# Optimization experiments

Measured on AMD Instinct MI355X. Metric: run time of the kernel, lower is better.

The kernel has to match this reference:

```python
import jax, jax.numpy as jnp
import numpy as np

B, E, L = 8, 512, 8192
MAX_W = 4          # max_subword_block_width -> widths 1..3
KSIZE = 5          # conv_kernel_size
DS = 2             # downsample_rate


def setup_inputs() -> dict:
    key = jax.random.key(0)
    k0, k1, k2, k3 = jax.random.split(key, 4)
    x = jax.random.normal(k0, (B, E, L), dtype=jnp.float32)
    # Conv1d(E, E, KSIZE): weight [out_ch, in_ch, k], bias [out_ch]
    conv_w = jax.random.normal(k1, (E, E, KSIZE), dtype=jnp.float32) * (1.0 / np.sqrt(E * KSIZE))
    conv_b = jax.random.normal(k2, (E,), dtype=jnp.float32) * 0.01
    # Linear(E, 1, bias=False): stored as vector [E]
    score_w = jax.random.normal(k3, (E,), dtype=jnp.float32) * (1.0 / np.sqrt(E))
    return {"x": x, "conv_w": conv_w, "conv_b": conv_b, "score_w": score_w}


def reference(x, conv_w, conv_b, score_w):
    length = x.shape[-1]  # original length, captured BEFORE the valid conv (as in torch)
    # Pre-GBST conv, VALID padding -> length shrinks by KSIZE-1
    y = jax.lax.conv_general_dilated(
        x, conv_w, window_strides=(1,), padding="VALID",
        dimension_numbers=("NCH", "OIH", "NCH"))
    y = y + conv_b[None, :, None]

    seqs, scs = [], []
    for w in range(1, MAX_W):
        Lc = y.shape[-1]
        pad = (-Lc) % w
        yp = jnp.pad(y, ((0, 0), (0, 0), (0, pad))) if pad else y
        # avg_pool1d(kernel=w, stride=w) == reshape + mean (zero-pad counts in mean, matching torch)
        cand = yp.reshape(yp.shape[0], yp.shape[1], -1, w).mean(-1)  # [B,E,Nb]
        sc = jnp.einsum("ben,e->bn", cand, score_w)                  # [B,Nb]
        rs = jnp.repeat(cand, w, axis=-1)  # [B,E,Nb*w]
        rc = jnp.repeat(sc, w, axis=-1)    # [B,Nb*w]
        Lr = rs.shape[-1]
        if Lr < length:
            rs = jnp.pad(rs, ((0, 0), (0, 0), (0, length - Lr)))
            rc = jnp.pad(rc, ((0, 0), (0, length - Lr)))
        seqs.append(rs[:, :, :length])
        scs.append(rc[:, :length])
    seqs = jnp.stack(seqs, axis=-1)            # [B,E,L,W-1]
    scs = jnp.stack(scs, axis=-1)[:, None]     # [B,1,L,W-1]
    att = jax.nn.softmax(scs, axis=-1)
    out = (seqs * att).sum(-1)                 # [B,E,L]
    # Downsample via avg_pool1d(kernel=DS, stride=DS)
    b, e, l = out.shape
    out = out[:, :, :(l // DS) * DS].reshape(b, e, l // DS, DS).mean(-1)
    return out
```

## Files before the change

### kernel.cpp

```cpp
#include <hip/hip_runtime.h>
#include <math.h>

#define B_    8
#define E_    512
#define L_    8192
#define K_    5
#define LC    8188
#define LOUT  4096
#define XROWS 8200
#define LCP   8208


typedef float  f32x4   __attribute__((ext_vector_type(4)));
typedef float  f32x16  __attribute__((ext_vector_type(16)));
typedef short  s16x4   __attribute__((ext_vector_type(4)));
typedef short  s16x8   __attribute__((ext_vector_type(8)));

__device__ __forceinline__ unsigned short f2bf(float f) {
    union { float f; unsigned u; } v; v.f = f;
    unsigned r = v.u + 0x7FFFu + ((v.u >> 16) & 1u);
    return (unsigned short)(r >> 16);
}
__device__ __forceinline__ float bflo(unsigned u) {
    union { unsigned u; float f; } v; v.u = u << 16; return v.f;
}
__device__ __forceinline__ float bfhi(unsigned u) {
    union { unsigned u; float f; } v; v.u = u & 0xFFFF0000u; return v.f;
}

__global__ __launch_bounds__(256) void wt_kernel(const float* __restrict__ w,
                                                 unsigned short* __restrict__ Wtb) {
    int idx = blockIdx.x * 256 + threadIdx.x;
    if (idx >= E_ * E_ * K_) return;
    int i    = idx & (E_ - 1);
    int rest = idx >> 9;
    int e    = rest & (E_ - 1);
    int k    = rest >> 9;
    Wtb[idx] = f2bf(w[((size_t)e * E_ + i) * K_ + k]);
}

__global__ __launch_bounds__(256) void xt_kernel(const float* __restrict__ x,
                                                 unsigned short* __restrict__ xT) {
    __shared__ float s[64][65];
    const int b  = blockIdx.z;
    const int i0 = blockIdx.y * 64;
    const int t0 = blockIdx.x * 64;
    #pragma unroll
    for (int j = 0; j < 4; ++j) {
        int idx = threadIdx.x + j * 256;
        int r = idx >> 4, c4 = idx & 15;
        f32x4 v = *(const f32x4*)(x + ((size_t)b * E_ + i0 + r) * L_ + t0 + c4 * 4);
        s[c4 * 4 + 0][r] = v[0];
        s[c4 * 4 + 1][r] = v[1];
        s[c4 * 4 + 2][r] = v[2];
        s[c4 * 4 + 3][r] = v[3];
    }
    __syncthreads();
    #pragma unroll
    for (int j = 0; j < 4; ++j) {
        int idx = threadIdx.x + j * 256;
        int tt = idx >> 4, ig = (idx & 15) * 4;
        s16x4 v;
        v[0] = (short)f2bf(s[tt][ig + 0]);
        v[1] = (short)f2bf(s[tt][ig + 1]);
        v[2] = (short)f2bf(s[tt][ig + 2]);
        v[3] = (short)f2bf(s[tt][ig + 3]);
        *(s16x4*)&xT[((size_t)b * XROWS + t0 + tt) * E_ + i0 + ig] = v;
    }
}

__global__ __launch_bounds__(256) void zero_aux(unsigned short* __restrict__ yP,
                                                float* __restrict__ zP) {
    int idx = blockIdx.x * 256 + threadIdx.x;
    if (idx < B_ * LCP) zP[idx] = 0.f;
    int i2 = idx - B_ * LCP;
    if (i2 >= 0 && i2 < B_ * E_ * 20) {
        int row = i2 / 20, j = i2 - row * 20;
        int col = (j < 8) ? j : (8 + LC + (j - 8));
        yP[(size_t)row * LCP + col] = 0;
    }
}

__global__ __launch_bounds__(256, 2) void conv_mfma(const unsigned short* __restrict__ xT,
                                                    const unsigned short* __restrict__ Wtb,
                                                    const float* __restrict__ bias,
                                                    const float* __restrict__ sw,
                                                    unsigned short* __restrict__ yP,
                                                    float* __restrict__ zP) {
    __shared__ unsigned short Xs[520][40];
    __shared__ unsigned short Ws[K_][64][40];
    __shared__ float swb[128];

    const int tid  = threadIdx.x;
    const int nt   = blockIdx.x;
    const int b    = nt >> 4;
    const int tb   = (nt & 15) * 512;
    const int e0   = blockIdx.y * 64;
    const int wave = tid >> 6;
    const int lane = tid & 63;
    const int l32  = lane & 31;
    const int hi   = lane >> 5;
    const int wt0  = wave * 128;

    if (tid < 64)       swb[tid] = sw[e0 + tid];
    else if (tid < 128) swb[tid] = bias[e0 + tid - 64];

    f32x16 acc[2][4];
    #pragma unroll
    for (int es = 0; es < 2; ++es)
        #pragma unroll
        for (int ts = 0; ts < 4; ++ts) acc[es][ts] = (f32x16)0.f;

    const unsigned short* xbase = xT + ((size_t)b * XROWS + tb) * E_;

    s16x8 xpf[9];
    s16x8 wpf[5];

    auto load_tile = [&](int i0) {
        #pragma unroll
        for (int j = 0; j < 8; ++j) {
            int idx = tid + j * 256;
            int r = idx >> 2, c = idx & 3;
            xpf[j] = *(const s16x8*)(xbase + (size_t)r * E_ + i0 + c * 8);
        }
        {
            int idx = tid + 2048;
            if (idx < 2080) {
                int r = idx >> 2, c = idx & 3;
                xpf[8] = *(const s16x8*)(xbase + (size_t)r * E_ + i0 + c * 8);
            }
        }
        #pragma unroll
        for (int j = 0; j < 5; ++j) {
            int idx = tid + j * 256;
            int rl = idx >> 2, c = idx & 3;
            int k = rl >> 6, ep = rl & 63;
            wpf[j] = *(const s16x8*)(Wtb + ((size_t)(k * E_ + e0 + ep) * E_ + i0 + c * 8));
        }
    };
    auto store_tile = [&]() {
        #pragma unroll
        for (int j = 0; j < 8; ++j) {
            int idx = tid + j * 256;
            int r = idx >> 2, c = idx & 3;
            *(s16x8*)&Xs[r][c * 8] = xpf[j];
        }
        {
            int idx = tid + 2048;
            if (idx < 2080) {
                int r = idx >> 2, c = idx & 3;
                *(s16x8*)&Xs[r][c * 8] = xpf[8];
            }
        }
        #pragma unroll
        for (int j = 0; j < 5; ++j) {
            int idx = tid + j * 256;
            int rl = idx >> 2, c = idx & 3;
            int k = rl >> 6, ep = rl & 63;
            *(s16x8*)&Ws[k][ep][c * 8] = wpf[j];
        }
    };

    load_tile(0);
    for (int i0 = 0; i0 < E_; i0 += 32) {
        __syncthreads();
        store_tile();
        __syncthreads();
        if (i0 + 32 < E_) load_tile(i0 + 32);

        #pragma unroll
        for (int k = 0; k < K_; ++k) {
            #pragma unroll
            for (int kk = 0; kk < 2; ++kk) {
                const int co = kk * 16 + hi * 8;
                s16x8 a0 = *(const s16x8*)&Ws[k][l32][co];
                s16x8 a1 = *(const s16x8*)&Ws[k][32 + l32][co];
                #pragma unroll
                for (int ts = 0; ts < 4; ++ts) {
                    s16x8 bv = *(const s16x8*)&Xs[wt0 + ts * 32 + l32 + k][co];
                    acc[0][ts] = __builtin_amdgcn_mfma_f32_32x32x16_bf16(a0, bv, acc[0][ts], 0, 0, 0);
                    acc[1][ts] = __builtin_amdgcn_mfma_f32_32x32x16_bf16(a1, bv, acc[1][ts], 0, 0, 0);
                }
            }
        }
    }

    #pragma unroll
    for (int ts = 0; ts < 4; ++ts) {
        const int t = tb + wt0 + ts * 32 + l32;
        const bool tv = (t < LC);
        float zp = 0.f;
        #pragma unroll
        for (int es = 0; es < 2; ++es) {
            #pragma unroll
            for (int reg = 0; reg < 16; ++reg) {
                int er = es * 32 + (reg & 3) + 8 * (reg >> 2) + 4 * hi;
                float v = acc[es][ts][reg] + swb[64 + er];
                if (tv) yP[((size_t)(b * E_ + e0 + er)) * LCP + 8 + t] = f2bf(v);
                zp += swb[er] * v;
            }
        }
        zp += __shfl_xor(zp, 32);
        if (hi == 0 && tv) atomicAdd(&zP[(size_t)b * LCP + 8 + t], zp);
    }
}

__global__ __launch_bounds__(256) void out3_kernel(const unsigned short* __restrict__ yP,
                                                   const float* __restrict__ zP,
                                                   float* __restrict__ out) {
    __shared__ float  zsL[1040];
    __shared__ float2 attA[512];
    __shared__ float2 attB[512];
    __shared__ float  attC[512];
    const int bx  = blockIdx.x;
    const int b   = bx >> 6;
    const int eg  = bx & 63;
    const int d0  = blockIdx.y << 9;
    const int tid = threadIdx.x;

    const float* zbase = zP + (size_t)b * LCP + 2 * d0;
    for (int c = tid; c < 260; c += 256)
        *(f32x4*)&zsL[c * 4] = *(const f32x4*)(zbase + c * 4);
    __syncthreads();

    for (int dl = tid; dl < 512; dl += 256) {
        int lt = 2 * dl + 6;
        float z0 = zsL[lt + 0], z1 = zsL[lt + 1], z2 = zsL[lt + 2];
        float z3 = zsL[lt + 3], z4 = zsL[lt + 4], z5 = zsL[lt + 5];
        unsigned t  = 2u * (unsigned)(d0 + dl);
        unsigned r3 = t % 3u;
        float a12 = z1 + z2, a34 = z3 + z4;
        float s0 = z0 + a12, s1 = a12 + z3, s2 = z2 + a34, s3 = a34 + z5;
        float S1a = z2, S1b = z3;
        float S2  = 0.5f * (z2 + z3);
        float S3a = ((r3 == 0u) ? s2 : ((r3 == 1u) ? s1 : s0)) * (1.f / 3.f);
        float S3b = ((r3 == 0u) ? s2 : ((r3 == 1u) ? s1 : s3)) * (1.f / 3.f);
        float m0 = fmaxf(S1a, fmaxf(S2, S3a));
        float e1 = __expf(S1a - m0), e2 = __expf(S2 - m0), e3 = __expf(S3a - m0);
        float r0 = 1.f / (e1 + e2 + e3);
        float m1 = fmaxf(S1b, fmaxf(S2, S3b));
        float f1 = __expf(S1b - m1), f2 = __expf(S2 - m1), f3 = __expf(S3b - m1);
        float r1 = 1.f / (f1 + f2 + f3);
        attA[dl] = make_float2(0.5f * e1 * r0, 0.5f * f1 * r1);
        attB[dl] = make_float2(0.25f * (e2 * r0 + f2 * r1), (0.5f / 3.f) * e3 * r0);
        attC[dl] = (0.5f / 3.f) * f3 * r1;
    }
    __syncthreads();

    const int e    = tid >> 5;
    const int l32b = tid & 31;
    const unsigned short* yrow = yP + ((size_t)(b * E_ + eg * 8 + e)) * LCP + 2 * d0;
    float* orow = out + ((size_t)(b * E_ + eg * 8 + e)) * LOUT + d0;
    #pragma unroll
    for (int ii = 0; ii < 16; ++ii) {
        int dl = l32b + 32 * ii;
        unsigned u0 = *(const unsigned*)(yrow + 2 * dl + 6);
        unsigned u1 = *(const unsigned*)(yrow + 2 * dl + 8);
        unsigned u2 = *(const unsigned*)(yrow + 2 * dl + 10);
        float v0 = bflo(u0), v1 = bfhi(u0);
        float v2 = bflo(u1), v3 = bfhi(u1);
        float v4 = bflo(u2), v5 = bfhi(u2);
        unsigned t  = 2u * (unsigned)(d0 + dl);
        unsigned r3 = t % 3u;
        float a12 = v1 + v2, a34 = v3 + v4;
        float s0 = v0 + a12, s1 = a12 + v3, s2 = v2 + a34, s3 = a34 + v5;
        float C3a = (r3 == 0u) ? s2 : ((r3 == 1u) ? s1 : s0);
        float C3b = (r3 == 0u) ? s2 : ((r3 == 1u) ? s1 : s3);
        float2 wA = attA[dl];
        float2 wB = attB[dl];
        float  wC = attC[dl];
        float o = wA.x * v2 + wA.y * v3 + wB.x * (v2 + v3) + wB.y * C3a + wC * C3b;
        orow[dl] = o;
    }
}

extern "C" void kernel_launch(void* const* d_in, const int* in_sizes, int n_in,
                              void* d_out, int out_size, void* d_ws, size_t ws_size,
                              hipStream_t stream) {
    const float* x       = (const float*)d_in[0];
    const float* conv_w  = (const float*)d_in[1];
    const float* conv_b  = (const float*)d_in[2];
    const float* score_w = (const float*)d_in[3];
    float* out = (float*)d_out;

    unsigned short* base = (unsigned short*)d_ws;
    unsigned short* Wtb = base;
    unsigned short* xT  = Wtb + (size_t)K_ * E_ * E_;
    unsigned short* yP  = xT + (size_t)B_ * XROWS * E_;
    float*          zP  = (float*)(yP + (size_t)B_ * E_ * LCP);

    wt_kernel<<<dim3((E_ * E_ * K_ + 255) / 256), 256, 0, stream>>>(conv_w, Wtb);
    xt_kernel<<<dim3(L_ / 64, E_ / 64, B_), 256, 0, stream>>>(x, xT);
    zero_aux<<<dim3((B_ * LCP + B_ * E_ * 20 + 255) / 256), 256, 0, stream>>>(yP, zP);
    conv_mfma<<<dim3(B_ * 16, E_ / 64), 256, 0, stream>>>(xT, Wtb, conv_b, score_w, yP, zP);
    out3_kernel<<<dim3(B_ * 64, LOUT / 512), 256, 0, stream>>>(yP, zP, out);
}
```

Before: 411.6 us.

## Stage conv tiles via direct global-to-LDS loads with double buffering

Result: slower. 428.2 us (+4.0%).

```diff
diff --git a/kernel.cpp b/kernel.cpp
--- a/kernel.cpp
+++ b/kernel.cpp
@@ -10,6 +10,14 @@
 #define XROWS 8200
 #define LCP   8208
 
+#define XR      516
+#define PITCH   24
+#define XCH     1548
+#define WCH     960
+#define NCH     2508
+#define CPW     627
+#define BUFU    20064
+#define WOFF    12384
 
 typedef float  f32x4   __attribute__((ext_vector_type(4)));
 typedef float  f32x16  __attribute__((ext_vector_type(16)));
@@ -26,6 +34,12 @@
 }
 __device__ __forceinline__ float bfhi(unsigned u) {
     union { unsigned u; float f; } v; v.u = u & 0xFFFF0000u; return v.f;
+}
+
+__device__ __forceinline__ void gload16(const unsigned short* g, unsigned short* l) {
+    __builtin_amdgcn_global_load_lds(
+        (const __attribute__((address_space(1))) unsigned int*)g,
+        (__attribute__((address_space(3))) unsigned int*)l, 16, 0, 0);
 }
 
 __global__ __launch_bounds__(256) void wt_kernel(const float* __restrict__ w,
@@ -87,8 +101,7 @@
                                                     const float* __restrict__ sw,
                                                     unsigned short* __restrict__ yP,
                                                     float* __restrict__ zP) {
-    __shared__ unsigned short Xs[520][40];
-    __shared__ unsigned short Ws[K_][64][40];
+    __shared__ unsigned short SB[2][BUFU];
     __shared__ float swb[128];
 
     const int tid  = threadIdx.x;
@@ -112,77 +125,64 @@
         for (int ts = 0; ts < 4; ++ts) acc[es][ts] = (f32x16)0.f;
 
     const unsigned short* xbase = xT + ((size_t)b * XROWS + tb) * E_;
-
-    s16x8 xpf[9];
-    s16x8 wpf[5];
-
-    auto load_tile = [&](int i0) {
-        #pragma unroll
-        for (int j = 0; j < 8; ++j) {
-            int idx = tid + j * 256;
-            int r = idx >> 2, c = idx & 3;
-            xpf[j] = *(const s16x8*)(xbase + (size_t)r * E_ + i0 + c * 8);
+    const int cw = wave * CPW;
+
+    auto src = [&](int g, int i0) -> const unsigned short* {
+        if (g < XCH) {
+            int row = g / 3, slot = g - row * 3;
+            return xbase + (size_t)row * E_ + i0 + (slot < 2 ? slot * 8 : 0);
+        } else {
+            int wg = g - XCH;
+            int rowl = wg / 3, slot = wg - rowl * 3;
+            int k = rowl >> 6, ep = rowl & 63;
+            return Wtb + ((size_t)(k * E_ + e0 + ep) * E_ + i0 + (slot < 2 ? slot * 8 : 0));
+        }
+    };
+    auto stage = [&](int p, int i0) {
+        unsigned short* base = &SB[p][0];
+        #pragma unroll
+        for (int it = 0; it < 9; ++it) {
+            int g = cw + it * 64;
+            gload16(src(g + lane, i0), base + (size_t)g * 8);
         }
         {
-            int idx = tid + 2048;
-            if (idx < 2080) {
-                int r = idx >> 2, c = idx & 3;
-                xpf[8] = *(const s16x8*)(xbase + (size_t)r * E_ + i0 + c * 8);
+            int g = cw + 576;
+            if (lane < CPW - 576)
+                gload16(src(g + lane, i0), base + (size_t)g * 8);
+        }
+    };
+
+    stage(0, 0);
+    int p = 0;
+    for (int s = 0; s < 32; ++s) {
+        if (s + 1 < 32) {
+            stage(p ^ 1, (s + 1) * 16);
+            asm volatile("s_waitcnt vmcnt(10)" ::: "memory");
+        } else {
+            asm volatile("s_waitcnt vmcnt(0)" ::: "memory");
+        }
+        asm volatile("" ::: "memory");
+        __builtin_amdgcn_s_barrier();
+        asm volatile("" ::: "memory");
+
+        const unsigned short* Xb = &SB[p][0];
+        const unsigned short* Wb = &SB[p][WOFF];
+        #pragma unroll
+        for (int k = 0; k < K_; ++k) {
+            s16x8 a0 = *(const s16x8*)(Wb + (size_t)(k * 64 + l32) * PITCH + hi * 8);
+            s16x8 a1 = *(const s16x8*)(Wb + (size_t)(k * 64 + 32 + l32) * PITCH + hi * 8);
+            #pragma unroll
+            for (int ts = 0; ts < 4; ++ts) {
+                s16x8 bv = *(const s16x8*)(Xb + (size_t)(wt0 + ts * 32 + l32 + k) * PITCH + hi * 8);
+                acc[0][ts] = __builtin_amdgcn_mfma_f32_32x32x16_bf16(a0, bv, acc[0][ts], 0, 0, 0);
+                acc[1][ts] = __builtin_amdgcn_mfma_f32_32x32x16_bf16(a1, bv, acc[1][ts], 0, 0, 0);
             }
         }
-        #pragma unroll
-        for (int j = 0; j < 5; ++j) {
-            int idx = tid + j * 256;
-            int rl = idx >> 2, c = idx & 3;
-            int k = rl >> 6, ep = rl & 63;
-            wpf[j] = *(const s16x8*)(Wtb + ((size_t)(k * E_ + e0 + ep) * E_ + i0 + c * 8));
-        }
-    };
-    auto store_tile = [&]() {
-        #pragma unroll
-        for (int j = 0; j < 8; ++j) {
-            int idx = tid + j * 256;
-            int r = idx >> 2, c = idx & 3;
-            *(s16x8*)&Xs[r][c * 8] = xpf[j];
-        }
-        {
-            int idx = tid + 2048;
-            if (idx < 2080) {
-                int r = idx >> 2, c = idx & 3;
-                *(s16x8*)&Xs[r][c * 8] = xpf[8];
-            }
-        }
-        #pragma unroll
-        for (int j = 0; j < 5; ++j) {
-            int idx = tid + j * 256;
-            int rl = idx >> 2, c = idx & 3;
-            int k = rl >> 6, ep = rl & 63;
-            *(s16x8*)&Ws[k][ep][c * 8] = wpf[j];
-        }
-    };
-
-    load_tile(0);
-    for (int i0 = 0; i0 < E_; i0 += 32) {
-        __syncthreads();
-        store_tile();
-        __syncthreads();
-        if (i0 + 32 < E_) load_tile(i0 + 32);
-
-        #pragma unroll
-        for (int k = 0; k < K_; ++k) {
-            #pragma unroll
-            for (int kk = 0; kk < 2; ++kk) {
-                const int co = kk * 16 + hi * 8;
-                s16x8 a0 = *(const s16x8*)&Ws[k][l32][co];
-                s16x8 a1 = *(const s16x8*)&Ws[k][32 + l32][co];
-                #pragma unroll
-                for (int ts = 0; ts < 4; ++ts) {
-                    s16x8 bv = *(const s16x8*)&Xs[wt0 + ts * 32 + l32 + k][co];
-                    acc[0][ts] = __builtin_amdgcn_mfma_f32_32x32x16_bf16(a0, bv, acc[0][ts], 0, 0, 0);
-                    acc[1][ts] = __builtin_amdgcn_mfma_f32_32x32x16_bf16(a1, bv, acc[1][ts], 0, 0, 0);
-                }
-            }
-        }
+
+        asm volatile("" ::: "memory");
+        __builtin_amdgcn_s_barrier();
+        asm volatile("" ::: "memory");
+        p ^= 1;
     }
 
     #pragma unroll
```
